# Optimization experiments

Measured on AMD Instinct MI355X. Metric: run time of the kernel, lower is better.

## Reference

```python
import jax, jax.numpy as jnp
import numpy as np

B, T_DEC, T_ENC = 64, 400, 512
D = 256    # embed_size (GRU units, attention units, attention_layer_size)
PRE = 128  # prenet output dim (Tacotron prenet: 256 -> 128)
OUT = 400  # n_mels * r = 80 * 5


def _p(k, shape, s=0.05):
    return jax.random.normal(k, shape, dtype=jnp.float32) * s


def setup_inputs() -> dict:
    ks = jax.random.split(jax.random.key(0), 16)
    return {
        "dec_inputs": jax.random.normal(ks[0], (B, T_DEC, OUT), dtype=jnp.float32),
        "memory": jax.random.normal(ks[1], (B, T_ENC, D), dtype=jnp.float32),
        "W1": _p(ks[2], (OUT, D)), "b1": jnp.zeros((D,), jnp.float32),
        "W2": _p(ks[3], (D, PRE)), "b2": jnp.zeros((PRE,), jnp.float32),
        "k0": _p(ks[4], (PRE + D, 3 * D)), "r0": _p(ks[5], (D, 3 * D)),
        "bi0": jnp.zeros((3 * D,), jnp.float32), "br0": jnp.zeros((3 * D,), jnp.float32),
        "k1": _p(ks[6], (D, 3 * D)), "r1": _p(ks[7], (D, 3 * D)),
        "bi1": jnp.zeros((3 * D,), jnp.float32), "br1": jnp.zeros((3 * D,), jnp.float32),
        "Wq": _p(ks[8], (D, D)), "Wm": _p(ks[9], (D, D)), "v": _p(ks[10], (D,)),
        "Wa": _p(ks[11], (2 * D, D)),
        "Wo": _p(ks[12], (D, OUT)), "bo": jnp.zeros((OUT,), jnp.float32),
    }


def _gru(x, h, Wk, Wr, bi, br):
    # Keras GRUCell (reset_after=True)
    gx = x @ Wk + bi
    gh = h @ Wr + br
    xz, xr, xh = jnp.split(gx, 3, axis=-1)
    hz, hr, hh = jnp.split(gh, 3, axis=-1)
    z = jax.nn.sigmoid(xz + hz)
    r = jax.nn.sigmoid(xr + hr)
    hcand = jnp.tanh(xh + r * hh)
    return z * h + (1.0 - z) * hcand


def reference(dec_inputs, memory, W1, b1, W2, b2, k0, r0, bi0, br0,
              k1, r1, bi1, br1, Wq, Wm, v, Wa, Wo, bo):
    # Prenet (teacher forcing -> can apply to all steps up front). Dropout is
    # identity in eval mode.
    p = jax.nn.relu(jax.nn.relu(dec_inputs @ W1 + b1) @ W2 + b2)  # [B,Td,PRE]
    keys = memory @ Wm  # Bahdanau memory layer, precomputed  [B,Te,D]
    b = dec_inputs.shape[0]
    h0 = jnp.zeros((b, D), dec_inputs.dtype)
    h1 = jnp.zeros((b, D), dec_inputs.dtype)
    att0 = jnp.zeros((b, D), dec_inputs.dtype)

    def step(carry, x):
        h0, h1, att = carry
        cin = jnp.concatenate([x, att], axis=-1)           # [B, PRE+D]
        h0n = _gru(cin, h0, k0, r0, bi0, br0)
        h1n = _gru(h0n, h1, k1, r1, bi1, br1)              # cell output
        q = h1n @ Wq                                        # query layer
        score = jnp.einsum('btd,d->bt', jnp.tanh(keys + q[:, None, :]), v)
        alpha = jax.nn.softmax(score, axis=-1)              # [B,Te]
        ctx = jnp.einsum('bt,btd->bd', alpha, memory)       # context
        attn = jnp.concatenate([h1n, ctx], axis=-1) @ Wa    # attention layer
        y = attn @ Wo + bo                                  # output Dense
        return (h0n, h1n, attn), y

    _, ys = jax.lax.scan(step, (h0, h1, att0), jnp.swapaxes(p, 0, 1))
    return jnp.swapaxes(ys, 0, 1)  # [B, T_DEC, OUT]
```

## Files before the change

### kernel.cpp

```cpp
#include <hip/hip_runtime.h>
#include <hip/hip_fp16.h>

#define BB   64
#define TDEC 400
#define TENC 512
#define DD   256
#define PRE  128
#define NOUT 400
#define G3   768
#define C2E  2.8853900817779268f

typedef _Float16 h2_t __attribute__((ext_vector_type(2)));

__device__ __forceinline__ float fsig(float x) {
    return __builtin_amdgcn_rcpf(1.0f + __expf(-x));
}
__device__ __forceinline__ float ftanh(float x) {
    float t = __expf(2.0f * x);
    return 1.0f - 2.0f * __builtin_amdgcn_rcpf(t + 1.0f);
}
__device__ __forceinline__ float fexp2(float x) {
#if __has_builtin(__builtin_amdgcn_exp2f)
    return __builtin_amdgcn_exp2f(x);
#else
    return exp2f(x);
#endif
}
__device__ __forceinline__ float dot8(float4 w, float4 x, float acc) {
    union { float4 f; h2_t h[4]; } uw, ux;
    uw.f = w; ux.f = x;
#if __has_builtin(__builtin_amdgcn_fdot2)
    #pragma unroll
    for (int k = 0; k < 4; k++)
        acc = __builtin_amdgcn_fdot2(uw.h[k], ux.h[k], acc, false);
#else
    #pragma unroll
    for (int k = 0; k < 4; k++) {
        acc = fmaf((float)uw.h[k].x, (float)ux.h[k].x, acc);
        acc = fmaf((float)uw.h[k].y, (float)ux.h[k].y, acc);
    }
#endif
    return acc;
}

__global__ __launch_bounds__(256) void prenet_kernel(
    const float* __restrict__ x, const float* __restrict__ W1, const float* __restrict__ b1,
    const float* __restrict__ W2, const float* __restrict__ b2, __half* __restrict__ p_h)
{
    __shared__ __align__(16) float xs[8][NOUT];
    __shared__ __align__(16) float hs[8][DD];
    const int row0 = blockIdx.x * 8;
    const int tid = threadIdx.x;
    for (int idx = tid; idx < 8 * NOUT; idx += 256) {
        int m = idx / NOUT, i = idx - m * NOUT;
        xs[m][i] = x[(size_t)(row0 + m) * NOUT + i];
    }
    __syncthreads();
    {
        const int j = tid;
        float acc[8];
        float bj = b1[j];
        #pragma unroll
        for (int m = 0; m < 8; m++) acc[m] = bj;
        #pragma unroll 4
        for (int i = 0; i < NOUT; i++) {
            float w = W1[i * DD + j];
            #pragma unroll
            for (int m = 0; m < 8; m++) acc[m] = fmaf(xs[m][i], w, acc[m]);
        }
        #pragma unroll
        for (int m = 0; m < 8; m++) hs[m][j] = fmaxf(acc[m], 0.0f);
    }
    __syncthreads();
    if (tid < PRE) {
        const int j = tid;
        float acc[8];
        float bj = b2[j];
        #pragma unroll
        for (int m = 0; m < 8; m++) acc[m] = bj;
        #pragma unroll 4
        for (int i = 0; i < DD; i++) {
            float w = W2[i * PRE + j];
            #pragma unroll
            for (int m = 0; m < 8; m++) acc[m] = fmaf(hs[m][i], w, acc[m]);
        }
        #pragma unroll
        for (int m = 0; m < 8; m++)
            p_h[(size_t)(row0 + m) * PRE + j] = __float2half(fmaxf(acc[m], 0.0f));
    }
}

__global__ __launch_bounds__(768) void gx0_kernel(
    const __half* __restrict__ p_h, const float* __restrict__ k0,
    const float* __restrict__ bi0, __half* __restrict__ gxp)
{
    __shared__ __align__(16) float ps[8][PRE];
    const int row0 = blockIdx.x * 8;
    const int tid = threadIdx.x;
    for (int idx = tid; idx < 8 * PRE; idx += 768) {
        int m = idx >> 7, i = idx & 127;
        ps[m][i] = __half2float(p_h[(size_t)(row0 + m) * PRE + i]);
    }
    __syncthreads();
    const int j = tid;
    float acc[8];
    float bj = bi0[j];
    #pragma unroll
    for (int m = 0; m < 8; m++) acc[m] = bj;
    #pragma unroll 4
    for (int i = 0; i < PRE; i++) {
        float w = k0[(size_t)i * G3 + j];
        #pragma unroll
        for (int m = 0; m < 8; m++) acc[m] = fmaf(ps[m][i], w, acc[m]);
    }
    #pragma unroll
    for (int m = 0; m < 8; m++)
        gxp[(size_t)(row0 + m) * G3 + j] = __float2half(acc[m]);
}

__global__ __launch_bounds__(256) void keys_kernel(
    const float* __restrict__ mem, const float* __restrict__ Wm, __half* __restrict__ keys_p)
{
    __shared__ __align__(16) float xs[8][DD];
    const int row0 = blockIdx.x * 8;
    const int tid = threadIdx.x;
    for (int idx = tid; idx < 8 * DD; idx += 256) {
        int m = idx >> 8, i = idx & 255;
        xs[m][i] = mem[(size_t)(row0 + m) * DD + i];
    }
    __syncthreads();
    const int j = tid;
    const int i8 = j >> 3, k = j & 7;
    float acc[8] = {0.f,0.f,0.f,0.f,0.f,0.f,0.f,0.f};
    #pragma unroll 4
    for (int i = 0; i < DD; i++) {
        float w = Wm[i * DD + j];
        #pragma unroll
        for (int m = 0; m < 8; m++) acc[m] = fmaf(xs[m][i], w, acc[m]);
    }
    #pragma unroll
    for (int m = 0; m < 8; m++) {
        int r = row0 + m;
        int bb = r >> 9, e = r & 511;
        keys_p[(size_t)bb * (TENC * DD) + ((size_t)i8 * TENC + e) * 8 + k] =
            __float2half(C2E * acc[m]);
    }
}

__global__ __launch_bounds__(256) void pack_w_kernel(
    const float* __restrict__ src, __half* __restrict__ dst, int R, int C)
{
    int flat = blockIdx.x * 256 + threadIdx.x;
    if (flat < R * C) {
        int k = flat & 7;
        int t2 = flat >> 3;
        int j = t2 % C;
        int i8 = t2 / C;
        dst[flat] = __float2half(src[(size_t)(8 * i8 + k) * C + j]);
    }
}

__global__ __launch_bounds__(256) void pack_mem_kernel(
    const float* __restrict__ mem, __half2* __restrict__ dst)
{
    int flat = blockIdx.x * 256 + threadIdx.x;
    if (flat < BB * 256 * 256) {
        int d  = flat & 255;
        int e2 = (flat >> 8) & 255;
        int b  = flat >> 16;
        const float* base = mem + ((size_t)b * TENC + 2 * e2) * DD + d;
        dst[flat] = __floats2half2_rn(base[0], base[DD]);
    }
}

__global__ __launch_bounds__(448) void out_kernel(
    const __half* __restrict__ ah, const float* __restrict__ Wo, const float* __restrict__ bo,
    float* __restrict__ y)
{
    __shared__ __align__(16) float xs[8][DD];
    const int row0 = blockIdx.x * 8;
    const int tid = threadIdx.x;
    for (int idx = tid; idx < 8 * DD; idx += 448) {
        int m = idx >> 8, i = idx & 255;
        xs[m][i] = __half2float(ah[(size_t)(row0 + m) * DD + i]);
    }
    __syncthreads();
    if (tid < NOUT) {
        const int j = tid;
        float acc[8];
        float bj = bo[j];
        #pragma unroll
        for (int m = 0; m < 8; m++) acc[m] = bj;
        #pragma unroll 4
        for (int i = 0; i < DD; i++) {
            float w = Wo[i * NOUT + j];
            #pragma unroll
            for (int m = 0; m < 8; m++) acc[m] = fmaf(xs[m][i], w, acc[m]);
        }
        #pragma unroll
        for (int m = 0; m < 8; m++) y[(size_t)(row0 + m) * NOUT + j] = acc[m];
    }
}

__global__ __launch_bounds__(768) void decoder_kernel(
    const __half* __restrict__ gxp,  const __half* __restrict__ keys_p,
    const __half2* __restrict__ mem_p,
    const __half* __restrict__ k0p,  const __half* __restrict__ r0p,
    const __half* __restrict__ k1p,  const __half* __restrict__ r1p,
    const __half* __restrict__ Wqp,  const __half* __restrict__ Wap,
    const float* __restrict__ br0,
    const float* __restrict__ bi1, const float* __restrict__ br1,
    const float* __restrict__ v,   __half* __restrict__ ahist)
{
    __shared__ __align__(16) __half xa[DD];
    __shared__ __align__(16) __half h0s[DD], h1s[DD];
    __shared__ __align__(16) __half ctxh[DD];
    __shared__ __align__(16) float h0f[DD], h1f[DD];
    __shared__ __align__(16) float qf[DD], vf[DD];
    __shared__ __align__(16) float gx[G3], gh[G3];
    __shared__ __align__(16) float sc[TENC];
    __shared__ __align__(16) float hWa[DD];
    __shared__ __align__(16) float ctxp[3][DD];
    __shared__ __align__(16) float b0r[G3], b1i[G3], b1r[G3];
    __shared__ __align__(16) float redd[16];
    __shared__ float svs;

    const int tid = threadIdx.x;
    const int b = blockIdx.x;

    b0r[tid] = br0[tid]; b1i[tid] = bi1[tid]; b1r[tid] = br1[tid];
    if (tid < DD) {
        h0f[tid] = 0.0f; h1f[tid] = 0.0f;
        h0s[tid] = __float2half(0.0f); h1s[tid] = __float2half(0.0f);
        vf[tid] = v[tid];
        xa[tid] = __float2half(0.0f);
    }
    __syncthreads();
    if (tid == 0) {
        float s = 0.0f;
        for (int i = 0; i < DD; i++) s += vf[i];
        svs = s;
    }
    const __half*  keyb = keys_p + (size_t)b * TENC * DD;
    const __half2* memb = mem_p + (size_t)b * (TENC / 2) * DD;
    const __half*  gxb  = gxp + (size_t)b * TDEC * G3;
    __half gpre = gxb[tid];
    __syncthreads();

    #pragma unroll 1
    for (int t = 0; t < TDEC; t++) {
        {
            float acc = __half2float(gpre);
            if (t + 1 < TDEC) gpre = gxb[(size_t)(t + 1) * G3 + tid];
            float acc2 = b0r[tid];
            const float4* wpA = (const float4*)k0p;
            const float4* wpB = (const float4*)r0p;
            const float4* xp  = (const float4*)xa;
            const float4* hp  = (const float4*)h0s;
            #pragma unroll 4
            for (int i8 = 0; i8 < 32; i8++) {
                acc  = dot8(wpA[(16 + i8) * G3 + tid], xp[i8], acc);
                acc2 = dot8(wpB[i8 * G3 + tid], hp[i8], acc2);
            }
            gx[tid] = acc; gh[tid] = acc2;
        }
        __syncthreads();
        if (tid < DD) {
            float z = fsig(gx[tid] + gh[tid]);
            float r = fsig(gx[DD + tid] + gh[DD + tid]);
            float cand = ftanh(gx[2 * DD + tid] + r * gh[2 * DD + tid]);
            float hn = z * h0f[tid] + (1.0f - z) * cand;
            h0f[tid] = hn; h0s[tid] = __float2half(hn);
        }
        __syncthreads();

        {
            const float4* wpA = (const float4*)k1p;
            const float4* wpB = (const float4*)r1p;
            const float4* xp  = (const float4*)h0s;
            const float4* hp  = (const float4*)h1s;
            float acc = b1i[tid], acc2 = b1r[tid];
            #pragma unroll 4
            for (int i8 = 0; i8 < 32; i8++) {
                acc  = dot8(wpA[i8 * G3 + tid], xp[i8], acc);
                acc2 = dot8(wpB[i8 * G3 + tid], hp[i8], acc2);
            }
            gx[tid] = acc; gh[tid] = acc2;
        }
        __syncthreads();
        if (tid < DD) {
            float z = fsig(gx[tid] + gh[tid]);
            float r = fsig(gx[DD + tid] + gh[DD + tid]);
            float cand = ftanh(gx[2 * DD + tid] + r * gh[2 * DD + tid]);
            float hn = z * h1f[tid] + (1.0f - z) * cand;
            h1f[tid] = hn; h1s[tid] = __float2half(hn);
        }
        __syncthreads();

        if (tid < DD) {
            const float4* wp = (const float4*)Wqp;
            const float4* hp = (const float4*)h1s;
            float acc = 0.0f;
            #pragma unroll 8
            for (int i8 = 0; i8 < 32; i8++) acc = dot8(wp[i8 * DD + tid], hp[i8], acc);
            qf[tid] = C2E * acc;
        }
        __syncthreads();

        if (tid < TENC) {
            const int e = tid;
            const float4* kp4 = (const float4*)keyb;
            const float4* qp4 = (const float4*)qf;
            const float4* vp4 = (const float4*)vf;
            float acc = 0.0f;
            #pragma unroll 4
            for (int i8 = 0; i8 < 32; i8++) {
                union { float4 f; h2_t h[4]; } uk;
                uk.f = kp4[i8 * TENC + e];
                float4 q0 = qp4[2 * i8], q1 = qp4[2 * i8 + 1];
                float4 v0 = vp4[2 * i8], v1 = vp4[2 * i8 + 1];
                float a0 = (float)uk.h[0].x + q0.x;
                float a1 = (float)uk.h[0].y + q0.y;
                float a2 = (float)uk.h[1].x + q0.z;
                float a3 = (float)uk.h[1].y + q0.w;
                float a4 = (float)uk.h[2].x + q1.x;
                float a5 = (float)uk.h[2].y + q1.y;
                float a6 = (float)uk.h[3].x + q1.z;
                float a7 = (float)uk.h[3].y + q1.w;
                acc = fmaf(v0.x, __builtin_amdgcn_rcpf(fexp2(a0) + 1.0f), acc);
                acc = fmaf(v0.y, __builtin_amdgcn_rcpf(fexp2(a1) + 1.0f), acc);
                acc = fmaf(v0.z, __builtin_amdgcn_rcpf(fexp2(a2) + 1.0f), acc);
                acc = fmaf(v0.w, __builtin_amdgcn_rcpf(fexp2(a3) + 1.0f), acc);
                acc = fmaf(v1.x, __builtin_amdgcn_rcpf(fexp2(a4) + 1.0f), acc);
                acc = fmaf(v1.y, __builtin_amdgcn_rcpf(fexp2(a5) + 1.0f), acc);
                acc = fmaf(v1.z, __builtin_amdgcn_rcpf(fexp2(a6) + 1.0f), acc);
                acc = fmaf(v1.w, __builtin_amdgcn_rcpf(fexp2(a7) + 1.0f), acc);
            }
            float s = svs - 2.0f * acc;
            float wv = __expf(s);
            sc[e] = wv;
            #pragma unroll
            for (int off = 32; off; off >>= 1) wv += __shfl_down(wv, off);
            if ((tid & 63) == 0) redd[tid >> 6] = wv;
        } else {
            const int d = tid - TENC;
            const float4* wp = (const float4*)Wap;
            const float4* hp = (const float4*)h1s;
            float acc = 0.0f;
            #pragma unroll 8
            for (int i8 = 0; i8 < 32; i8++) acc = dot8(wp[i8 * DD + d], hp[i8], acc);
            hWa[d] = acc;
        }
        __syncthreads();

        {
            const int d  = tid & 255;
            const int ch = tid >> 8;
            const int e8s = (ch == 0) ? 0 : (ch == 1) ? 22 : 43;
            const int e8e = (ch == 0) ? 22 : (ch == 1) ? 43 : 64;
            const float4* scp = (const float4*)sc;
            float acc = 0.0f;
            #pragma unroll 2
            for (int e8 = e8s; e8 < e8e; e8++) {
                float4 w0 = scp[2 * e8], w1 = scp[2 * e8 + 1];
                __half2 m0 = memb[(4 * e8 + 0) * DD + d];
                __half2 m1 = memb[(4 * e8 + 1) * DD + d];
                __half2 m2 = memb[(4 * e8 + 2) * DD + d];
                __half2 m3 = memb[(4 * e8 + 3) * DD + d];
                float2 f0 = __half22float2(m0), f1 = __half22float2(m1);
                float2 f2 = __half22float2(m2), f3 = __half22float2(m3);
                acc = fmaf(f0.x, w0.x, acc); acc = fmaf(f0.y, w0.y, acc);
                acc = fmaf(f1.x, w0.z, acc); acc = fmaf(f1.y, w0.w, acc);
                acc = fmaf(f2.x, w1.x, acc); acc = fmaf(f2.y, w1.y, acc);
                acc = fmaf(f3.x, w1.z, acc); acc = fmaf(f3.y, w1.w, acc);
            }
            ctxp[ch][d] = acc;
        }
        __syncthreads();

        if (tid < DD) {
            const float4* rp = (const float4*)redd;
            float4 ra = rp[0], rb = rp[1];
            float ssum = ((ra.x + ra.y) + (ra.z + ra.w)) + ((rb.x + rb.y) + (rb.z + rb.w));
            float c = (ctxp[0][tid] + ctxp[1][tid] + ctxp[2][tid]) * __builtin_amdgcn_rcpf(ssum);
            ctxh[tid] = __float2half(c);
        }
        __syncthreads();

        if (tid < DD) {
            const float4* wp = (const float4*)Wap;
            const float4* cp = (const float4*)ctxh;
            float acc = hWa[tid];
            #pragma unroll 8
            for (int i8 = 0; i8 < 32; i8++) acc = dot8(wp[(32 + i8) * DD + tid], cp[i8], acc);
            __half ah = __float2half(acc);
            xa[tid] = ah;
            ahist[((size_t)b * TDEC + t) * DD + tid] = ah;
        }
        __syncthreads();
    }
}

extern "C" void kernel_launch(void* const* d_in, const int* in_sizes, int n_in,
                              void* d_out, int out_size, void* d_ws, size_t ws_size,
                              hipStream_t stream)
{
    const float* dec    = (const float*)d_in[0];
    const float* memory = (const float*)d_in[1];
    const float* W1  = (const float*)d_in[2];
    const float* b1  = (const float*)d_in[3];
    const float* W2  = (const float*)d_in[4];
    const float* b2  = (const float*)d_in[5];
    const float* k0  = (const float*)d_in[6];
    const float* r0  = (const float*)d_in[7];
    const float* bi0 = (const float*)d_in[8];
    const float* br0 = (const float*)d_in[9];
    const float* k1  = (const float*)d_in[10];
    const float* r1  = (const float*)d_in[11];
    const float* bi1 = (const float*)d_in[12];
    const float* br1 = (const float*)d_in[13];
    const float* Wq  = (const float*)d_in[14];
    const float* Wm  = (const float*)d_in[15];
    const float* v   = (const float*)d_in[16];
    const float* Wa  = (const float*)d_in[17];
    const float* Wo  = (const float*)d_in[18];
    const float* bo  = (const float*)d_in[19];
    float* out = (float*)d_out;
    (void)ws_size; (void)in_sizes; (void)n_in; (void)out_size;

    char* w = (char*)d_ws;
    size_t off = 0;
    __half*  p_h    = (__half*)(w + off);  off += (size_t)BB * TDEC * PRE * 2;
    __half*  keys_p = (__half*)(w + off);  off += (size_t)BB * TENC * DD * 2;
    __half2* mem_p  = (__half2*)(w + off); off += (size_t)BB * TENC * DD * 2;
    __half*  gxp    = (__half*)(w + off);  off += (size_t)BB * TDEC * G3 * 2;
    __half*  k0p    = (__half*)(w + off);  off += (size_t)384 * G3 * 2;
    __half*  r0p    = (__half*)(w + off);  off += (size_t)DD * G3 * 2;
    __half*  k1p    = (__half*)(w + off);  off += (size_t)DD * G3 * 2;
    __half*  r1p    = (__half*)(w + off);  off += (size_t)DD * G3 * 2;
    __half*  Wqp    = (__half*)(w + off);  off += (size_t)DD * DD * 2;
    __half*  Wap    = (__half*)(w + off);  off += (size_t)2 * DD * DD * 2;
    __half*  ahist  = (__half*)(w + off);  off += (size_t)BB * TDEC * DD * 2;

    prenet_kernel<<<BB * TDEC / 8, 256, 0, stream>>>(dec, W1, b1, W2, b2, p_h);
    gx0_kernel<<<BB * TDEC / 8, 768, 0, stream>>>(p_h, k0, bi0, gxp);
    keys_kernel<<<BB * TENC / 8, 256, 0, stream>>>(memory, Wm, keys_p);
    pack_mem_kernel<<<(BB * 256 * 256) / 256, 256, 0, stream>>>(memory, mem_p);
    pack_w_kernel<<<(384 * G3 + 255) / 256, 256, 0, stream>>>(k0, k0p, 384, G3);
    pack_w_kernel<<<(DD * G3 + 255) / 256, 256, 0, stream>>>(r0, r0p, DD, G3);
    pack_w_kernel<<<(DD * G3 + 255) / 256, 256, 0, stream>>>(k1, k1p, DD, G3);
    pack_w_kernel<<<(DD * G3 + 255) / 256, 256, 0, stream>>>(r1, r1p, DD, G3);
    pack_w_kernel<<<(DD * DD + 255) / 256, 256, 0, stream>>>(Wq, Wqp, DD, DD);
    pack_w_kernel<<<(2 * DD * DD + 255) / 256, 256, 0, stream>>>(Wa, Wap, 2 * DD, DD);

    decoder_kernel<<<BB, 768, 0, stream>>>(gxp, keys_p, mem_p, k0p, r0p, k1p, r1p,
                                           Wqp, Wap, br0, bi1, br1, v, ahist);

    out_kernel<<<BB * TDEC / 8, 448, 0, stream>>>(ahist, Wo, bo, out);
}
```

Baseline: 14.91 ms.

## Shrink decoder block to 512 threads and cache attention keys in registers

The recurrent decoder block shrinks from 768 to 512 threads, and each thread keeps its encoder key row in registers for all steps instead of reloading keys every step. The 768-wide GRU gate columns are now split unevenly, with 256 threads doing a second column. The query and Wa projections of h1 are computed together in one phase, which removes one barrier. The constant sum(v) term in the score is dropped because it cancels in the softmax, and the accumulator chains are split in two for more instruction-level parallelism. The costs are heavy register pressure (128 VGPRs for keys under a 512x2 launch bound, so spills are possible), imbalanced GRU work across threads, and a possible overflow in exp without the shift.

Result: slower. 41.77 ms (+180.2%).

```diff
diff --git a/kernel.cpp b/kernel.cpp
--- a/kernel.cpp
+++ b/kernel.cpp
@@ -202,7 +202,7 @@
     }
 }
 
-__global__ __launch_bounds__(768) void decoder_kernel(
+__global__ __launch_bounds__(512, 2) void decoder_kernel(
     const __half* __restrict__ gxp,  const __half* __restrict__ keys_p,
     const __half2* __restrict__ mem_p,
     const __half* __restrict__ k0p,  const __half* __restrict__ r0p,
@@ -220,49 +220,67 @@
     __shared__ __align__(16) float gx[G3], gh[G3];
     __shared__ __align__(16) float sc[TENC];
     __shared__ __align__(16) float hWa[DD];
-    __shared__ __align__(16) float ctxp[3][DD];
+    __shared__ __align__(16) float ctxp[2][DD];
     __shared__ __align__(16) float b0r[G3], b1i[G3], b1r[G3];
     __shared__ __align__(16) float redd[16];
-    __shared__ float svs;
 
     const int tid = threadIdx.x;
     const int b = blockIdx.x;
 
-    b0r[tid] = br0[tid]; b1i[tid] = bi1[tid]; b1r[tid] = br1[tid];
+    for (int i = tid; i < G3; i += 512) {
+        b0r[i] = br0[i]; b1i[i] = bi1[i]; b1r[i] = br1[i];
+    }
     if (tid < DD) {
         h0f[tid] = 0.0f; h1f[tid] = 0.0f;
         h0s[tid] = __float2half(0.0f); h1s[tid] = __float2half(0.0f);
         vf[tid] = v[tid];
         xa[tid] = __float2half(0.0f);
     }
-    __syncthreads();
-    if (tid == 0) {
-        float s = 0.0f;
-        for (int i = 0; i < DD; i++) s += vf[i];
-        svs = s;
-    }
     const __half*  keyb = keys_p + (size_t)b * TENC * DD;
     const __half2* memb = mem_p + (size_t)b * (TENC / 2) * DD;
     const __half*  gxb  = gxp + (size_t)b * TDEC * G3;
-    __half gpre = gxb[tid];
+
+    float4 kreg[32];
+    #pragma unroll
+    for (int i8 = 0; i8 < 32; i8++)
+        kreg[i8] = ((const float4*)keyb)[i8 * TENC + tid];
+
+    __half gpre0 = gxb[tid];
+    __half gpre1 = (tid < 256) ? gxb[512 + tid] : __float2half(0.0f);
     __syncthreads();
 
     #pragma unroll 1
     for (int t = 0; t < TDEC; t++) {
         {
-            float acc = __half2float(gpre);
-            if (t + 1 < TDEC) gpre = gxb[(size_t)(t + 1) * G3 + tid];
-            float acc2 = b0r[tid];
             const float4* wpA = (const float4*)k0p;
             const float4* wpB = (const float4*)r0p;
             const float4* xp  = (const float4*)xa;
             const float4* hp  = (const float4*)h0s;
+            float accA  = __half2float(gpre0);
+            float acc2A = b0r[tid];
             #pragma unroll 4
             for (int i8 = 0; i8 < 32; i8++) {
-                acc  = dot8(wpA[(16 + i8) * G3 + tid], xp[i8], acc);
-                acc2 = dot8(wpB[i8 * G3 + tid], hp[i8], acc2);
-            }
-            gx[tid] = acc; gh[tid] = acc2;
+                float4 x = xp[i8], h = hp[i8];
+                accA  = dot8(wpA[(16 + i8) * G3 + tid], x, accA);
+                acc2A = dot8(wpB[i8 * G3 + tid], h, acc2A);
+            }
+            gx[tid] = accA; gh[tid] = acc2A;
+            if (tid < 256) {
+                const int j = 512 + tid;
+                float accB  = __half2float(gpre1);
+                float acc2B = b0r[j];
+                #pragma unroll 4
+                for (int i8 = 0; i8 < 32; i8++) {
+                    float4 x = xp[i8], h = hp[i8];
+                    accB  = dot8(wpA[(16 + i8) * G3 + j], x, accB);
+                    acc2B = dot8(wpB[i8 * G3 + j], h, acc2B);
+                }
+                gx[j] = accB; gh[j] = acc2B;
+            }
+            if (t + 1 < TDEC) {
+                gpre0 = gxb[(size_t)(t + 1) * G3 + tid];
+                if (tid < 256) gpre1 = gxb[(size_t)(t + 1) * G3 + 512 + tid];
+            }
         }
         __syncthreads();
         if (tid < DD) {
@@ -279,13 +297,27 @@
             const float4* wpB = (const float4*)r1p;
             const float4* xp  = (const float4*)h0s;
             const float4* hp  = (const float4*)h1s;
-            float acc = b1i[tid], acc2 = b1r[tid];
+            float accA  = b1i[tid];
+            float acc2A = b1r[tid];
             #pragma unroll 4
             for (int i8 = 0; i8 < 32; i8++) {
-                acc  = dot8(wpA[i8 * G3 + tid], xp[i8], acc);
-                acc2 = dot8(wpB[i8 * G3 + tid], hp[i8], acc2);
-            }
-            gx[tid] = acc; gh[tid] = acc2;
+                float4 x = xp[i8], h = hp[i8];
+                accA  = dot8(wpA[i8 * G3 + tid], x, accA);
+                acc2A = dot8(wpB[i8 * G3 + tid], h, acc2A);
+            }
+            gx[tid] = accA; gh[tid] = acc2A;
+            if (tid < 256) {
+                const int j = 512 + tid;
+                float accB  = b1i[j];
+                float acc2B = b1r[j];
+                #pragma unroll 4
+                for (int i8 = 0; i8 < 32; i8++) {
+                    float4 x = xp[i8], h = hp[i8];
+                    accB  = dot8(wpA[i8 * G3 + j], x, accB);
+                    acc2B = dot8(wpB[i8 * G3 + j], h, acc2B);
+                }
+                gx[j] = accB; gh[j] = acc2B;
+            }
         }
         __syncthreads();
         if (tid < DD) {
@@ -297,26 +329,38 @@
         }
         __syncthreads();
 
-        if (tid < DD) {
+        if (tid < 256) {
             const float4* wp = (const float4*)Wqp;
             const float4* hp = (const float4*)h1s;
-            float acc = 0.0f;
-            #pragma unroll 8
-            for (int i8 = 0; i8 < 32; i8++) acc = dot8(wp[i8 * DD + tid], hp[i8], acc);
-            qf[tid] = C2E * acc;
-        }
-        __syncthreads();
-
-        if (tid < TENC) {
-            const int e = tid;
-            const float4* kp4 = (const float4*)keyb;
+            float a0 = 0.0f, a1 = 0.0f;
+            #pragma unroll 4
+            for (int i8 = 0; i8 < 32; i8 += 2) {
+                a0 = dot8(wp[i8 * DD + tid], hp[i8], a0);
+                a1 = dot8(wp[(i8 + 1) * DD + tid], hp[i8 + 1], a1);
+            }
+            qf[tid] = C2E * (a0 + a1);
+        } else {
+            const int d = tid - 256;
+            const float4* wp = (const float4*)Wap;
+            const float4* hp = (const float4*)h1s;
+            float a0 = 0.0f, a1 = 0.0f;
+            #pragma unroll 4
+            for (int i8 = 0; i8 < 32; i8 += 2) {
+                a0 = dot8(wp[i8 * DD + d], hp[i8], a0);
+                a1 = dot8(wp[(i8 + 1) * DD + d], hp[i8 + 1], a1);
+            }
+            hWa[d] = a0 + a1;
+        }
+        __syncthreads();
+
+        {
             const float4* qp4 = (const float4*)qf;
             const float4* vp4 = (const float4*)vf;
-            float acc = 0.0f;
-            #pragma unroll 4
+            float accA = 0.0f, accB = 0.0f;
+            #pragma unroll
             for (int i8 = 0; i8 < 32; i8++) {
                 union { float4 f; h2_t h[4]; } uk;
-                uk.f = kp4[i8 * TENC + e];
+                uk.f = kreg[i8];
                 float4 q0 = qp4[2 * i8], q1 = qp4[2 * i8 + 1];
                 float4 v0 = vp4[2 * i8], v1 = vp4[2 * i8 + 1];
                 float a0 = (float)uk.h[0].x + q0.x;
@@ -327,41 +371,30 @@
                 float a5 = (float)uk.h[2].y + q1.y;
                 float a6 = (float)uk.h[3].x + q1.z;
                 float a7 = (float)uk.h[3].y + q1.w;
-                acc = fmaf(v0.x, __builtin_amdgcn_rcpf(fexp2(a0) + 1.0f), acc);
-                acc = fmaf(v0.y, __builtin_amdgcn_rcpf(fexp2(a1) + 1.0f), acc);
-                acc = fmaf(v0.z, __builtin_amdgcn_rcpf(fexp2(a2) + 1.0f), acc);
-                acc = fmaf(v0.w, __builtin_amdgcn_rcpf(fexp2(a3) + 1.0f), acc);
-                acc = fmaf(v1.x, __builtin_amdgcn_rcpf(fexp2(a4) + 1.0f), acc);
-                acc = fmaf(v1.y, __builtin_amdgcn_rcpf(fexp2(a5) + 1.0f), acc);
-                acc = fmaf(v1.z, __builtin_amdgcn_rcpf(fexp2(a6) + 1.0f), acc);
-                acc = fmaf(v1.w, __builtin_amdgcn_rcpf(fexp2(a7) + 1.0f), acc);
-            }
-            float s = svs - 2.0f * acc;
-            float wv = __expf(s);
-            sc[e] = wv;
+                accA = fmaf(v0.x, __builtin_amdgcn_rcpf(fexp2(a0) + 1.0f), accA);
+                accB = fmaf(v0.y, __builtin_amdgcn_rcpf(fexp2(a1) + 1.0f), accB);
+                accA = fmaf(v0.z, __builtin_amdgcn_rcpf(fexp2(a2) + 1.0f), accA);
+                accB = fmaf(v0.w, __builtin_amdgcn_rcpf(fexp2(a3) + 1.0f), accB);
+                accA = fmaf(v1.x, __builtin_amdgcn_rcpf(fexp2(a4) + 1.0f), accA);
+                accB = fmaf(v1.y, __builtin_amdgcn_rcpf(fexp2(a5) + 1.0f), accB);
+                accA = fmaf(v1.z, __builtin_amdgcn_rcpf(fexp2(a6) + 1.0f), accA);
+                accB = fmaf(v1.w, __builtin_amdgcn_rcpf(fexp2(a7) + 1.0f), accB);
+            }
+            float wv = __expf(-2.0f * (accA + accB));
+            sc[tid] = wv;
             #pragma unroll
             for (int off = 32; off; off >>= 1) wv += __shfl_down(wv, off);
             if ((tid & 63) == 0) redd[tid >> 6] = wv;
-        } else {
-            const int d = tid - TENC;
-            const float4* wp = (const float4*)Wap;
-            const float4* hp = (const float4*)h1s;
-            float acc = 0.0f;
-            #pragma unroll 8
-            for (int i8 = 0; i8 < 32; i8++) acc = dot8(wp[i8 * DD + d], hp[i8], acc);
-            hWa[d] = acc;
         }
         __syncthreads();
 
         {
             const int d  = tid & 255;
             const int ch = tid >> 8;
-            const int e8s = (ch == 0) ? 0 : (ch == 1) ? 22 : 43;
-            const int e8e = (ch == 0) ? 22 : (ch == 1) ? 43 : 64;
             const float4* scp = (const float4*)sc;
             float acc = 0.0f;
             #pragma unroll 2
-            for (int e8 = e8s; e8 < e8e; e8++) {
+            for (int e8 = ch * 32; e8 < ch * 32 + 32; e8++) {
                 float4 w0 = scp[2 * e8], w1 = scp[2 * e8 + 1];
                 __half2 m0 = memb[(4 * e8 + 0) * DD + d];
                 __half2 m1 = memb[(4 * e8 + 1) * DD + d];
@@ -382,7 +415,7 @@
             const float4* rp = (const float4*)redd;
             float4 ra = rp[0], rb = rp[1];
             float ssum = ((ra.x + ra.y) + (ra.z + ra.w)) + ((rb.x + rb.y) + (rb.z + rb.w));
-            float c = (ctxp[0][tid] + ctxp[1][tid] + ctxp[2][tid]) * __builtin_amdgcn_rcpf(ssum);
+            float c = (ctxp[0][tid] + ctxp[1][tid]) * __builtin_amdgcn_rcpf(ssum);
             ctxh[tid] = __float2half(c);
         }
         __syncthreads();
@@ -390,10 +423,13 @@
         if (tid < DD) {
             const float4* wp = (const float4*)Wap;
             const float4* cp = (const float4*)ctxh;
-            float acc = hWa[tid];
-            #pragma unroll 8
-            for (int i8 = 0; i8 < 32; i8++) acc = dot8(wp[(32 + i8) * DD + tid], cp[i8], acc);
-            __half ah = __float2half(acc);
+            float a0 = hWa[tid], a1 = 0.0f;
+            #pragma unroll 4
+            for (int i8 = 0; i8 < 32; i8 += 2) {
+                a0 = dot8(wp[(32 + i8) * DD + tid], cp[i8], a0);
+                a1 = dot8(wp[(33 + i8) * DD + tid], cp[i8 + 1], a1);
+            }
+            __half ah = __float2half(a0 + a1);
             xa[tid] = ah;
             ahist[((size_t)b * TDEC + t) * DD + tid] = ah;
         }
@@ -453,7 +489,7 @@
     pack_w_kernel<<<(DD * DD + 255) / 256, 256, 0, stream>>>(Wq, Wqp, DD, DD);
     pack_w_kernel<<<(2 * DD * DD + 255) / 256, 256, 0, stream>>>(Wa, Wap, 2 * DD, DD);
 
-    decoder_kernel<<<BB, 768, 0, stream>>>(gxp, keys_p, mem_p, k0p, r0p, k1p, r1p,
+    decoder_kernel<<<BB, 512, 0, stream>>>(gxp, keys_p, mem_p, k0p, r0p, k1p, r1p,
                                            Wqp, Wap, br0, bi1, br1, v, ahist);
 
     out_kernel<<<BB * TDEC / 8, 448, 0, stream>>>(ahist, Wo, bo, out);
```
